# Kernel tuning notes

Measured on AMD Instinct MI355X. Metric: run time of the kernel, lower is better.

Reference implementation:

```python
import jax, jax.numpy as jnp
import numpy as np

B, N = 1, 768
CM, CP = 384, 128            # msa_channel (single repr), pair_channel
H, SQK, SV, PQK, PV = 12, 16, 16, 4, 8
NOUT = 384
NFIN = H * SV + H * PV * 4 + H * CP  # 2112
FP16_HUGE = 65504.0
DIST_EPS = 1e-8


def _quat_to_rot(q):
    # normalized quaternion [B,N,4] -> rotation matrix [B,N,3,3]
    q = q / jnp.sqrt(jnp.sum(q * q, axis=-1, keepdims=True))
    w, x, y, z = q[..., 0], q[..., 1], q[..., 2], q[..., 3]
    return jnp.stack([
        jnp.stack([1 - 2 * (y * y + z * z), 2 * (x * y - w * z), 2 * (x * z + w * y)], -1),
        jnp.stack([2 * (x * y + w * z), 1 - 2 * (x * x + z * z), 2 * (y * z - w * x)], -1),
        jnp.stack([2 * (x * z - w * y), 2 * (y * z + w * x), 1 - 2 * (x * x + y * y)], -1),
    ], -2)


def setup_inputs() -> dict:
    key = jax.random.key(0)
    ks = jax.random.split(key, 20)
    s = 0.02
    return {
        'inputs_1d': jax.random.normal(ks[0], (B, N, CM), jnp.float32),
        'inputs_2d': jax.random.normal(ks[1], (B, N, N, CP), jnp.float32),
        'mask': jnp.ones((B, N, 1), jnp.float32),
        'quat': jax.random.normal(ks[2], (B, N, 4), jnp.float32),
        'trans': jax.random.normal(ks[3], (B, N, 3), jnp.float32),
        'wq': jax.random.normal(ks[4], (CM, H * SQK), jnp.float32) * s,
        'bq': jnp.zeros((H * SQK,), jnp.float32),
        'wkv': jax.random.normal(ks[5], (CM, H * (SQK + SV)), jnp.float32) * s,
        'bkv': jnp.zeros((H * (SQK + SV),), jnp.float32),
        'wqp': jax.random.normal(ks[6], (CM, H * 3 * PQK), jnp.float32) * s,
        'bqp': jnp.zeros((H * 3 * PQK,), jnp.float32),
        'wkvp': jax.random.normal(ks[7], (CM, H * 3 * (PQK + PV)), jnp.float32) * s,
        'bkvp': jnp.zeros((H * 3 * (PQK + PV),), jnp.float32),
        'pw_raw': jnp.full((H,), 0.541323855, jnp.float32),
        'w2d': jax.random.normal(ks[8], (CP, H), jnp.float32) * s,
        'b2d': jnp.zeros((H,), jnp.float32),
        'wout': jax.random.normal(ks[9], (NFIN, NOUT), jnp.float32) * s,
        'bout': jnp.zeros((NOUT,), jnp.float32),
    }


def _ipa(inputs_1d, inputs_2d, mask, quat, trans,
         wq, bq, wkv, bkv, wqp, bqp, wkvp, bkvp, pw_raw, w2d, b2d, wout, bout):
    R = _quat_to_rot(quat)                      # [B,N,3,3]

    # --- scalar q/k/v ---
    q_s = (inputs_1d @ wq + bq).reshape(B, N, H, SQK)
    kv_s = (inputs_1d @ wkv + bkv).reshape(B, N, H, SQK + SV)
    k_s, v_s = kv_s[..., :SQK], kv_s[..., SQK:]

    # --- point q/k/v in global frame: R @ p_local + t ---
    qp = (inputs_1d @ wqp + bqp).reshape(B, N, 3, H * PQK)  # split order: x,y,z blocks
    qp_g = jnp.einsum('bnij,bnjp->bnip', R, qp) + trans[..., None]
    kvp = (inputs_1d @ wkvp + bkvp).reshape(B, N, 3, H * (PQK + PV))
    kvp_g = (jnp.einsum('bnij,bnjp->bnip', R, kvp) + trans[..., None]
             ).reshape(B, N, 3, H, PQK + PV)
    kp_g, vp_g = kvp_g[..., :PQK], kvp_g[..., PQK:]

    # --- attention weights ---
    scalar_w = (1.0 / (3.0 * SQK)) ** 0.5
    point_w = ((1.0 / (3.0 * PQK * 4.5)) ** 0.5) * jax.nn.softplus(pw_raw)  # [H]

    # point-distance logits: -0.5*w_h * sum_{xyz,p} (q-k)^2, via |q|^2+|k|^2-2qk
    q_pt = jnp.transpose(qp_g.reshape(B, N, 3, H, PQK), (0, 3, 1, 2, 4)).reshape(B, H, N, 3 * PQK)
    k_pt = jnp.transpose(kp_g, (0, 3, 1, 2, 4)).reshape(B, H, N, 3 * PQK)
    qq = jnp.sum(q_pt * q_pt, -1)               # [B,H,N]
    kk = jnp.sum(k_pt * k_pt, -1)
    cross = jnp.einsum('bhnd,bhmd->bhnm', q_pt, k_pt)
    attn_pt = -0.5 * point_w[None, :, None, None] * (
        qq[..., :, None] + kk[..., None, :] - 2.0 * cross)

    attn_sc = jnp.einsum('bnhd,bmhd->bhnm', q_s * scalar_w, k_s)
    a2d = jnp.transpose(inputs_2d @ w2d + b2d, (0, 3, 1, 2)) * (1.0 / 3.0) ** 0.5

    logits = attn_sc + attn_pt + a2d
    mask2d = mask * jnp.swapaxes(mask, -1, -2)  # [B,N,N]
    logits = logits - FP16_HUGE * (1.0 - mask2d[:, None])
    attn = jax.nn.softmax(logits, axis=-1)      # [B,H,N,N]

    # --- aggregation ---
    res_s = jnp.einsum('bhnm,bmhd->bnhd', attn, v_s).reshape(B, N, H * SV)
    v_pt = jnp.transpose(vp_g, (0, 3, 1, 2, 4)).reshape(B, H, N, 3 * PV)
    res_pt_g = jnp.einsum('bhnm,bhmd->bhnd', attn, v_pt).reshape(B, H, N, 3, PV)
    res_pt_g = jnp.transpose(res_pt_g, (0, 2, 3, 1, 4)).reshape(B, N, 3, H * PV)
    # invert point: R^T (g - t)
    res_pt_l = jnp.einsum('bnji,bnjp->bnip', R, res_pt_g - trans[..., None])  # [B,N,3,H*PV]
    pt_norm = jnp.sqrt(DIST_EPS + jnp.sum(res_pt_l * res_pt_l, axis=2))       # [B,N,H*PV]
    res_2d = jnp.einsum('bhnm,bnmc->bnhc', attn, inputs_2d).reshape(B, N, H * CP)

    final = jnp.concatenate(
        [res_s, res_pt_l[:, :, 0], res_pt_l[:, :, 1], res_pt_l[:, :, 2], pt_norm, res_2d], -1)
    return final @ wout + bout


def reference(inputs_1d, inputs_2d, mask, quat, trans,
              wq, bq, wkv, bkv, wqp, bqp, wkvp, bkvp, pw_raw, w2d, b2d, wout, bout):
    return _ipa(inputs_1d, inputs_2d, mask, quat, trans,
                wq, bq, wkv, bkv, wqp, bqp, wkvp, bkvp, pw_raw, w2d, b2d, wout, bout)
```

## Files before the change

### kernel.cpp

```cpp
#include <hip/hip_runtime.h>
#include <cstdint>
#include <cstddef>

static constexpr float SCALAR_W = 0.14433756729740643f;
static constexpr float PTW_C    = 0.13608276348795434f;
static constexpr float RSQRT3   = 0.5773502691896258f;
static constexpr float FP16HUGE = 65504.0f;

static constexpr size_t OFF_P    = 0;
static constexpr size_t OFF_R    = 884736;
static constexpr size_t OFF_QPG  = 891648;
static constexpr size_t OFF_KVPG = 1002240;
static constexpr size_t OFF_LG   = 1334016;
static constexpr size_t OFF_FIN  = 8633088;
static constexpr size_t OFF_VCAT = 10255104;
static constexpr size_t OFF_KST  = 10623744;
static constexpr size_t OFF_KPT  = 10771200;
static constexpr size_t WS_TOTAL = 10881792;

__global__ void k_sentinel(float* __restrict__ out, int nel, float val)
{
    const int i = blockIdx.x * 256 + threadIdx.x;
    if (i < nel) out[i] = val;
}

__global__ __launch_bounds__(256) void k_proj_all(const float* __restrict__ A,
    const float* __restrict__ wq,  const float* __restrict__ bq,
    const float* __restrict__ wkv, const float* __restrict__ bkv,
    const float* __restrict__ wqp, const float* __restrict__ bqp,
    const float* __restrict__ wkvp,const float* __restrict__ bkvp,
    float* __restrict__ P)
{
    const int z = blockIdx.z;
    const float* Bm; const float* bias; int ncols, colbase;
    switch (z) {
        case 0: Bm = wq;   bias = bq;   ncols = 192; colbase = 0;   break;
        case 1: Bm = wkv;  bias = bkv;  ncols = 384; colbase = 192; break;
        case 2: Bm = wqp;  bias = bqp;  ncols = 144; colbase = 576; break;
        default:Bm = wkvp; bias = bkvp; ncols = 432; colbase = 720; break;
    }
    if (blockIdx.x * 256 >= ncols) return;
    __shared__ float At[8][384];
    const int t = threadIdx.x;
    const int r0 = blockIdx.y * 8;
    const float4* A4 = reinterpret_cast<const float4*>(A + (size_t)r0 * 384);
    float4* At4 = reinterpret_cast<float4*>(&At[0][0]);
#pragma unroll
    for (int i = 0; i < 3; ++i) At4[t + 256 * i] = A4[t + 256 * i];
    __syncthreads();
    const int col = blockIdx.x * 256 + t;
    if (col >= ncols) return;
    float acc[8] = {0.f,0.f,0.f,0.f,0.f,0.f,0.f,0.f};
    const float* bp = Bm + col;
#pragma unroll 4
    for (int k = 0; k < 384; ++k) {
        const float b = bp[(size_t)k * ncols];
#pragma unroll
        for (int r = 0; r < 8; ++r) acc[r] += At[r][k] * b;
    }
    const float bb = bias[col];
#pragma unroll
    for (int r = 0; r < 8; ++r)
        P[(size_t)(r0 + r) * 1152 + colbase + col] = acc[r] + bb;
}

__global__ __launch_bounds__(256) void k_rmat(const float* __restrict__ quat,
    float* __restrict__ ws)
{
    const int o = blockIdx.x * 256 + threadIdx.x;
    if (o >= 768 * 9) return;
    const int n = o / 9, e = o - 9 * n;
    const float q0 = quat[n*4+0], q1 = quat[n*4+1], q2 = quat[n*4+2], q3 = quat[n*4+3];
    const float inv = 1.0f / sqrtf(q0*q0 + q1*q1 + q2*q2 + q3*q3);
    const float w = q0*inv, x = q1*inv, y = q2*inv, z = q3*inv;
    float R[9];
    R[0] = 1.f - 2.f*(y*y + z*z); R[1] = 2.f*(x*y - w*z); R[2] = 2.f*(x*z + w*y);
    R[3] = 2.f*(x*y + w*z); R[4] = 1.f - 2.f*(x*x + z*z); R[5] = 2.f*(y*z - w*x);
    R[6] = 2.f*(x*z - w*y); R[7] = 2.f*(y*z + w*x); R[8] = 1.f - 2.f*(x*x + y*y);
    ws[OFF_R + o] = R[e];
}

__global__ __launch_bounds__(256) void k_rigid(const float* __restrict__ trans,
    float* __restrict__ ws)
{
    const int o = blockIdx.x * 256 + threadIdx.x;
    if (o >= 768 * 576) return;
    const int n = o / 576, e = o - 576 * n;
    const float* R = ws + OFF_R + (size_t)n * 9;
    if (e < 144) {
        const int i = e / 48, p = e - 48 * i;
        const float* Pn = ws + OFF_P + (size_t)n * 1152 + 576;
        ws[OFF_QPG + (size_t)n*144 + e] =
            R[i*3+0]*Pn[p] + R[i*3+1]*Pn[48+p] + R[i*3+2]*Pn[96+p] + trans[n*3+i];
    } else {
        const int e2 = e - 144;
        const int i = e2 / 144, p = e2 - 144 * i;
        const float* Pn = ws + OFF_P + (size_t)n * 1152 + 720;
        ws[OFF_KVPG + (size_t)n*432 + e2] =
            R[i*3+0]*Pn[p] + R[i*3+1]*Pn[144+p] + R[i*3+2]*Pn[288+p] + trans[n*3+i];
    }
}

__global__ __launch_bounds__(256) void k_vk(float* __restrict__ ws)
{
    const int o = blockIdx.x * 256 + threadIdx.x;
    if (o < 768 * 480) {
        const int m = o / 480, q = o - 480 * m;
        float v;
        if (q < 192) {
            const int h = q >> 4, d = q & 15;
            v = ws[OFF_P + (size_t)m*1152 + 192 + h*32 + 16 + d];
        } else {
            const int q2 = q - 192;
            const int i = q2 / 96, r = q2 - 96*i, h = r >> 3, c = r & 7;
            v = ws[OFF_KVPG + (size_t)m*432 + i*144 + h*12 + 4 + c];
        }
        ws[OFF_VCAT + o] = v;
    } else {
        const int o2 = o - 768 * 480;
        if (o2 >= 768 * 336) return;
        const int m = o2 / 336, q = o2 - 336 * m;
        if (q < 192) {
            const int h = q >> 4, k = q & 15;
            ws[OFF_KST + (size_t)(h*16 + k)*768 + m] =
                ws[OFF_P + (size_t)m*1152 + 192 + h*32 + k];
        } else {
            const int d2 = q - 192;
            const int h = d2 / 12, d = d2 - 12 * h;
            const int i = d >> 2, a = d & 3;
            ws[OFF_KPT + (size_t)(h*12 + d)*768 + m] =
                ws[OFF_KVPG + (size_t)m*432 + i*144 + h*12 + a];
        }
    }
}

__global__ __launch_bounds__(256) void k_lga(const float* __restrict__ in2d,
    const float* __restrict__ w2d, const float* __restrict__ b2d,
    const float* __restrict__ maskp, const float* __restrict__ pw_raw,
    float* __restrict__ ws)
{
    __shared__ float w2l[1536];
    __shared__ float a2l[12][260];
    __shared__ float qs[192], qpl[144], pwl[12], b2l[12];
    const int n = blockIdx.x, mt = blockIdx.y, t = threadIdx.x;
    if (t < 192) qs[t] = ws[OFF_P + (size_t)n*1152 + t] * SCALAR_W;
    if (t < 144) qpl[t] = ws[OFF_QPG + (size_t)n*144 + t];
    if (t < 12) {
        pwl[t] = PTW_C * logf(1.f + expf(pw_raw[t]));
        b2l[t] = b2d[t];
    }
    for (int i = t; i < 1536; i += 256) w2l[i] = w2d[i];
    const float mask_n = maskp[n];
    __syncthreads();

    const int cg = t & 3, pr = t >> 2;
    const int cg4 = cg * 4;
#pragma unroll
    for (int half = 0; half < 4; ++half) {
        const int mm = half * 64 + pr;
        const int m = mt * 256 + mm;
        const float* p = in2d + ((size_t)n * 768 + m) * 128;
        float acc[12] = {0,0,0,0,0,0,0,0,0,0,0,0};
#pragma unroll
        for (int cq = 0; cq < 8; ++cq) {
            const float4 v = *reinterpret_cast<const float4*>(p + cq * 16 + cg4);
#pragma unroll
            for (int j = 0; j < 4; ++j) {
                const float x = (&v.x)[j];
                const int c = cq * 16 + cg4 + j;
#pragma unroll
                for (int h = 0; h < 12; ++h) acc[h] += x * w2l[c * 12 + h];
            }
        }
#pragma unroll
        for (int h = 0; h < 12; ++h) {
            acc[h] += __shfl_xor(acc[h], 1);
            acc[h] += __shfl_xor(acc[h], 2);
        }
        if (cg == 0) {
#pragma unroll
            for (int h = 0; h < 12; ++h)
                a2l[h][mm] = (acc[h] + b2l[h]) * RSQRT3;
        }
    }
    __syncthreads();

    const float* kst = ws + OFF_KST;
    const float* kpt = ws + OFF_KPT;
    const int m = mt * 256 + t;
    const float pen = FP16HUGE * (1.f - mask_n * maskp[m]);
#pragma unroll
    for (int h = 0; h < 12; ++h) {
        float sc = 0.f;
        const float* ks = kst + (size_t)(h*16)*768 + m;
#pragma unroll
        for (int k = 0; k < 16; ++k) sc += qs[h*16 + k] * ks[(size_t)k*768];
        float d2 = 0.f;
        const float* kp = kpt + (size_t)(h*12)*768 + m;
#pragma unroll
        for (int d = 0; d < 12; ++d) {
            const int ii = d >> 2, a = d & 3;
            const float dq = qpl[ii*48 + h*4 + a] - kp[(size_t)d*768];
            d2 += dq * dq;
        }
        ws[OFF_LG + ((size_t)n * 12 + h) * 768 + m] =
            sc - 0.5f * pwl[h] * d2 - pen + a2l[h][t];
    }
}

__global__ __launch_bounds__(512) void k_att(const float* __restrict__ in2d,
    const float* __restrict__ trans, float* __restrict__ ws)
{
    __shared__ float at[12][776];
    __shared__ float part[4][1536];
    __shared__ float fl[480];
    __shared__ float ptl[288];
    __shared__ float Rl[9], trl[3];
    const int n = blockIdx.x, t = threadIdx.x;
    const int wv = t >> 6, lane = t & 63;
    if (t < 9) Rl[t] = ws[OFF_R + n*9 + t];
    if (t < 3) trl[t] = trans[n*3 + t];
    {
        const float4* a4 = reinterpret_cast<const float4*>(ws + OFF_LG + (size_t)n * 9216);
        for (int i = t; i < 2304; i += 512) {
            const int row = i / 192, j = i - row * 192;
            *reinterpret_cast<float4*>(&at[row][j * 4]) = a4[i];
        }
    }
    __syncthreads();

    for (int h = wv; h < 12; h += 8) {
        float v[12];
        float mx = -3.0e38f;
#pragma unroll
        for (int i = 0; i < 12; ++i) { v[i] = at[h][lane + i*64]; mx = fmaxf(mx, v[i]); }
#pragma unroll
        for (int off = 32; off > 0; off >>= 1) mx = fmaxf(mx, __shfl_xor(mx, off));
        float s = 0.f;
#pragma unroll
        for (int i = 0; i < 12; ++i) { v[i] = expf(v[i] - mx); s += v[i]; }
#pragma unroll
        for (int off = 32; off > 0; off >>= 1) s += __shfl_xor(s, off);
        const float inv = 1.f / s;
#pragma unroll
        for (int i = 0; i < 12; ++i) at[h][lane + i*64] = v[i] * inv;
    }
    __syncthreads();

    {
        const int c = t & 127, g = t >> 7;
        const float* p = in2d + (size_t)n * 768 * 128 + c;
        float acc[12] = {0,0,0,0,0,0,0,0,0,0,0,0};
        const int m0 = g * 192;
#pragma unroll 4
        for (int m = m0; m < m0 + 192; ++m) {
            const float x = p[(size_t)m * 128];
#pragma unroll
            for (int h = 0; h < 12; ++h) acc[h] += at[h][m] * x;
        }
#pragma unroll
        for (int h = 0; h < 12; ++h) part[g][h * 128 + c] = acc[h];
    }
    __syncthreads();
    {
        float* fo = ws + OFF_FIN + (size_t)n * 2112 + 576;
        for (int o = t; o < 1536; o += 512)
            fo[o] = part[0][o] + part[1][o] + part[2][o] + part[3][o];
    }

    if (t < 480) {
        int h;
        if (t < 192) h = t >> 4;
        else { const int r = (t - 192) % 96; h = r >> 3; }
        const float* v = ws + OFF_VCAT + t;
        const float* a = &at[h][0];
        float s = 0.f;
        for (int m = 0; m < 768; ++m) s += a[m] * v[(size_t)m * 480];
        fl[t] = s;
    }
    __syncthreads();

    float* fo = ws + OFF_FIN + (size_t)n * 2112;
    if (t < 192) fo[t] = fl[t];
    if (t < 288) {
        const int i = t / 96, p = t - 96 * i;
        float s = 0.f;
#pragma unroll
        for (int j = 0; j < 3; ++j)
            s += Rl[j*3 + i] * (fl[192 + j*96 + p] - trl[j]);
        fo[192 + t] = s;
        ptl[t] = s;
    }
    __syncthreads();
    if (t < 96) {
        const float a = ptl[t], b = ptl[96 + t], c = ptl[192 + t];
        fo[480 + t] = sqrtf(1e-8f + a*a + b*b + c*c);
    }
}

__global__ __launch_bounds__(256) void k_final(const float* __restrict__ wout,
    const float* __restrict__ bout, const float* __restrict__ ws,
    float* __restrict__ out)
{
    __shared__ float At[8][64];
    __shared__ float Bt[64][132];
    const float* fin = ws + OFF_FIN;
    const int r0 = blockIdx.y * 8;
    const int c0 = blockIdx.x * 128;
    const int t = threadIdx.x;
    const int c = t & 127, half = t >> 7;
    float acc[4] = {0.f, 0.f, 0.f, 0.f};
    for (int k0 = 0; k0 < 2112; k0 += 64) {
        __syncthreads();
        if (t < 128) {
            const int r = t >> 4, j = t & 15;
            *reinterpret_cast<float4*>(&At[r][j * 4]) =
                *reinterpret_cast<const float4*>(&fin[(size_t)(r0 + r) * 2112 + k0 + j * 4]);
        }
#pragma unroll
        for (int i = t; i < 2048; i += 256) {
            const int k = i >> 5, j = i & 31;
            *reinterpret_cast<float4*>(&Bt[k][j * 4]) =
                *reinterpret_cast<const float4*>(&wout[(size_t)(k0 + k) * 384 + c0 + j * 4]);
        }
        __syncthreads();
#pragma unroll
        for (int k = 0; k < 64; ++k) {
            const float b = Bt[k][c];
#pragma unroll
            for (int r = 0; r < 4; ++r) acc[r] += At[half*4 + r][k] * b;
        }
    }
#pragma unroll
    for (int r = 0; r < 4; ++r)
        out[(size_t)(r0 + half*4 + r) * 384 + c0 + c] = acc[r] + bout[c0 + c];
}

extern "C" void kernel_launch(void* const* d_in, const int* in_sizes, int n_in,
                              void* d_out, int out_size, void* d_ws, size_t ws_size,
                              hipStream_t stream)
{
    const float* in1d  = (const float*)d_in[0];
    const float* in2d  = (const float*)d_in[1];
    const float* maskp = (const float*)d_in[2];
    const float* quat  = (const float*)d_in[3];
    const float* trans = (const float*)d_in[4];
    const float* wq    = (const float*)d_in[5];
    const float* bq    = (const float*)d_in[6];
    const float* wkv   = (const float*)d_in[7];
    const float* bkv   = (const float*)d_in[8];
    const float* wqp   = (const float*)d_in[9];
    const float* bqp   = (const float*)d_in[10];
    const float* wkvp  = (const float*)d_in[11];
    const float* bkvp  = (const float*)d_in[12];
    const float* pwr   = (const float*)d_in[13];
    const float* w2d   = (const float*)d_in[14];
    const float* b2d   = (const float*)d_in[15];
    const float* wout  = (const float*)d_in[16];
    const float* bout  = (const float*)d_in[17];
    float* ws  = (float*)d_ws;
    float* out = (float*)d_out;

    if (ws_size < WS_TOTAL * sizeof(float)) {
        const float val = 1000.0f + (float)(ws_size / (1024.0 * 1024.0));
        k_sentinel<<<dim3((out_size + 255) / 256), dim3(256), 0, stream>>>(out, out_size, val);
        return;
    }

    dim3 blk(256);
    k_proj_all<<<dim3(2, 96, 4), blk, 0, stream>>>(in1d, wq, bq, wkv, bkv,
                                                   wqp, bqp, wkvp, bkvp, ws);
    k_rmat<<<dim3((768*9 + 255)/256), blk, 0, stream>>>(quat, ws);
    k_rigid<<<dim3((768*576 + 255)/256), blk, 0, stream>>>(trans, ws);
    k_vk<<<dim3((768*816 + 255)/256), blk, 0, stream>>>(ws);
    k_lga<<<dim3(768, 3), blk, 0, stream>>>(in2d, w2d, b2d, maskp, pwr, ws);
    k_att<<<dim3(768), dim3(512), 0, stream>>>(in2d, trans, ws);
    k_final<<<dim3(3, 96), blk, 0, stream>>>(wout, bout, ws, out);
}
```

Measured before the change: 495.2 us.

## Fuse logit computation into attention kernel, removing the logits workspace round trip

Merges the kernel that builds attention logits (pair bias, scalar and point terms) into the softmax/aggregation kernel, one block per query row with 512 threads. Logits are written straight into shared memory instead of a global buffer that was written and then re-read, and one kernel launch goes away. The cost is fewer blocks for the logit phase (768 instead of 2304) and higher shared-memory use per block, which may lower occupancy. The 2d input row of the same query is now read twice within one block, so the second read may hit in cache.

Result: slower. 932.7 us (+88.3%).

```diff
diff --git a/kernel.cpp b/kernel.cpp
--- a/kernel.cpp
+++ b/kernel.cpp
@@ -11,7 +11,6 @@
 static constexpr size_t OFF_R    = 884736;
 static constexpr size_t OFF_QPG  = 891648;
 static constexpr size_t OFF_KVPG = 1002240;
-static constexpr size_t OFF_LG   = 1334016;
 static constexpr size_t OFF_FIN  = 8633088;
 static constexpr size_t OFF_VCAT = 10255104;
 static constexpr size_t OFF_KST  = 10623744;
@@ -134,97 +133,87 @@
     }
 }
 
-__global__ __launch_bounds__(256) void k_lga(const float* __restrict__ in2d,
+__global__ __launch_bounds__(512) void k_fused(const float* __restrict__ in2d,
     const float* __restrict__ w2d, const float* __restrict__ b2d,
     const float* __restrict__ maskp, const float* __restrict__ pw_raw,
-    float* __restrict__ ws)
-{
+    const float* __restrict__ trans, float* __restrict__ ws)
+{
+    __shared__ float at[12][776];
+    __shared__ float part[4][1536];
     __shared__ float w2l[1536];
-    __shared__ float a2l[12][260];
     __shared__ float qs[192], qpl[144], pwl[12], b2l[12];
-    const int n = blockIdx.x, mt = blockIdx.y, t = threadIdx.x;
+    __shared__ float fl[480];
+    __shared__ float ptl[288];
+    __shared__ float Rl[9], trl[3];
+    const int n = blockIdx.x, t = threadIdx.x;
+    const int wv = t >> 6, lane = t & 63;
+
     if (t < 192) qs[t] = ws[OFF_P + (size_t)n*1152 + t] * SCALAR_W;
     if (t < 144) qpl[t] = ws[OFF_QPG + (size_t)n*144 + t];
     if (t < 12) {
         pwl[t] = PTW_C * logf(1.f + expf(pw_raw[t]));
         b2l[t] = b2d[t];
     }
-    for (int i = t; i < 1536; i += 256) w2l[i] = w2d[i];
-    const float mask_n = maskp[n];
-    __syncthreads();
-
-    const int cg = t & 3, pr = t >> 2;
-    const int cg4 = cg * 4;
-#pragma unroll
-    for (int half = 0; half < 4; ++half) {
-        const int mm = half * 64 + pr;
-        const int m = mt * 256 + mm;
-        const float* p = in2d + ((size_t)n * 768 + m) * 128;
-        float acc[12] = {0,0,0,0,0,0,0,0,0,0,0,0};
-#pragma unroll
-        for (int cq = 0; cq < 8; ++cq) {
-            const float4 v = *reinterpret_cast<const float4*>(p + cq * 16 + cg4);
-#pragma unroll
-            for (int j = 0; j < 4; ++j) {
-                const float x = (&v.x)[j];
-                const int c = cq * 16 + cg4 + j;
-#pragma unroll
-                for (int h = 0; h < 12; ++h) acc[h] += x * w2l[c * 12 + h];
-            }
-        }
-#pragma unroll
-        for (int h = 0; h < 12; ++h) {
-            acc[h] += __shfl_xor(acc[h], 1);
-            acc[h] += __shfl_xor(acc[h], 2);
-        }
-        if (cg == 0) {
-#pragma unroll
-            for (int h = 0; h < 12; ++h)
-                a2l[h][mm] = (acc[h] + b2l[h]) * RSQRT3;
-        }
-    }
-    __syncthreads();
-
-    const float* kst = ws + OFF_KST;
-    const float* kpt = ws + OFF_KPT;
-    const int m = mt * 256 + t;
-    const float pen = FP16HUGE * (1.f - mask_n * maskp[m]);
-#pragma unroll
-    for (int h = 0; h < 12; ++h) {
-        float sc = 0.f;
-        const float* ks = kst + (size_t)(h*16)*768 + m;
-#pragma unroll
-        for (int k = 0; k < 16; ++k) sc += qs[h*16 + k] * ks[(size_t)k*768];
-        float d2 = 0.f;
-        const float* kp = kpt + (size_t)(h*12)*768 + m;
-#pragma unroll
-        for (int d = 0; d < 12; ++d) {
-            const int ii = d >> 2, a = d & 3;
-            const float dq = qpl[ii*48 + h*4 + a] - kp[(size_t)d*768];
-            d2 += dq * dq;
-        }
-        ws[OFF_LG + ((size_t)n * 12 + h) * 768 + m] =
-            sc - 0.5f * pwl[h] * d2 - pen + a2l[h][t];
-    }
-}
-
-__global__ __launch_bounds__(512) void k_att(const float* __restrict__ in2d,
-    const float* __restrict__ trans, float* __restrict__ ws)
-{
-    __shared__ float at[12][776];
-    __shared__ float part[4][1536];
-    __shared__ float fl[480];
-    __shared__ float ptl[288];
-    __shared__ float Rl[9], trl[3];
-    const int n = blockIdx.x, t = threadIdx.x;
-    const int wv = t >> 6, lane = t & 63;
     if (t < 9) Rl[t] = ws[OFF_R + n*9 + t];
     if (t < 3) trl[t] = trans[n*3 + t];
+    for (int i = t; i < 1536; i += 512) w2l[i] = w2d[i];
+    const float mask_n = maskp[n];
+    __syncthreads();
+
     {
-        const float4* a4 = reinterpret_cast<const float4*>(ws + OFF_LG + (size_t)n * 9216);
-        for (int i = t; i < 2304; i += 512) {
-            const int row = i / 192, j = i - row * 192;
-            *reinterpret_cast<float4*>(&at[row][j * 4]) = a4[i];
+        const int cg = t & 3, pr = t >> 2;
+        const int cg4 = cg * 4;
+#pragma unroll 1
+        for (int r = 0; r < 6; ++r) {
+            const int m = r * 128 + pr;
+            const float* p = in2d + ((size_t)n * 768 + m) * 128;
+            float acc[12] = {0,0,0,0,0,0,0,0,0,0,0,0};
+#pragma unroll
+            for (int cq = 0; cq < 8; ++cq) {
+                const float4 v = *reinterpret_cast<const float4*>(p + cq * 16 + cg4);
+#pragma unroll
+                for (int j = 0; j < 4; ++j) {
+                    const float x = (&v.x)[j];
+                    const float* wr = &w2l[(cq * 16 + cg4 + j) * 12];
+#pragma unroll
+                    for (int h = 0; h < 12; ++h) acc[h] += x * wr[h];
+                }
+            }
+#pragma unroll
+            for (int h = 0; h < 12; ++h) {
+                acc[h] += __shfl_xor(acc[h], 1);
+                acc[h] += __shfl_xor(acc[h], 2);
+            }
+            if (cg == 0) {
+#pragma unroll
+                for (int h = 0; h < 12; ++h)
+                    at[h][m] = (acc[h] + b2l[h]) * RSQRT3;
+            }
+        }
+    }
+    __syncthreads();
+
+    {
+        const float* kst = ws + OFF_KST;
+        const float* kpt = ws + OFF_KPT;
+        for (int m = t; m < 768; m += 512) {
+            const float pen = FP16HUGE * (1.f - mask_n * maskp[m]);
+#pragma unroll
+            for (int h = 0; h < 12; ++h) {
+                float sc = 0.f;
+                const float* ks = kst + (size_t)(h*16)*768 + m;
+#pragma unroll
+                for (int k = 0; k < 16; ++k) sc += qs[h*16 + k] * ks[(size_t)k*768];
+                float d2 = 0.f;
+                const float* kp = kpt + (size_t)(h*12)*768 + m;
+#pragma unroll
+                for (int d = 0; d < 12; ++d) {
+                    const int ii = d >> 2, a = d & 3;
+                    const float dq = qpl[ii*48 + h*4 + a] - kp[(size_t)d*768];
+                    d2 += dq * dq;
+                }
+                at[h][m] += sc - 0.5f * pwl[h] * d2 - pen;
+            }
         }
     }
     __syncthreads();
@@ -373,7 +362,7 @@
     k_rmat<<<dim3((768*9 + 255)/256), blk, 0, stream>>>(quat, ws);
     k_rigid<<<dim3((768*576 + 255)/256), blk, 0, stream>>>(trans, ws);
     k_vk<<<dim3((768*816 + 255)/256), blk, 0, stream>>>(ws);
-    k_lga<<<dim3(768, 3), blk, 0, stream>>>(in2d, w2d, b2d, maskp, pwr, ws);
-    k_att<<<dim3(768), dim3(512), 0, stream>>>(in2d, trans, ws);
+    k_fused<<<dim3(768), dim3(512), 0, stream>>>(in2d, w2d, b2d, maskp, pwr,
+                                                 trans, ws);
     k_final<<<dim3(3, 96), blk, 0, stream>>>(wout, bout, ws, out);
 }
```

## Split logits kernel into reuse-tiled q·k/point-distance pass and pair-bias pass

Applied to the files above, without the earlier changes.

The fused logits kernel is split in two. k_log computes the scalar q·k and point-distance terms for 8 query rows per block, keeping each key column's 16 scalar and 12 point values in registers and reusing them across those 8 rows. This cuts global reads of the transposed key tensors by a factor of eight. k_a2d then streams the pair representation and adds the 2D bias into the logits with a read-modify-write, which costs an extra kernel launch and one more pass over the logits buffer.

New measurement: 495.6 us. No clear change (+0.1%).

```diff
diff --git a/kernel.cpp b/kernel.cpp
--- a/kernel.cpp
+++ b/kernel.cpp
@@ -134,23 +134,67 @@
     }
 }
 
-__global__ __launch_bounds__(256) void k_lga(const float* __restrict__ in2d,
+__global__ __launch_bounds__(256) void k_log(const float* __restrict__ maskp,
+    const float* __restrict__ pw_raw, float* __restrict__ ws)
+{
+    __shared__ float qsl[8][192], qpl8[8][144], pwl[12], mskn[8];
+    const int nt = blockIdx.x, mt = blockIdx.y, t = threadIdx.x;
+    const int n0 = nt * 8;
+    for (int idx = t; idx < 1536; idx += 256) {
+        const int i = idx / 192, j = idx - i * 192;
+        qsl[i][j] = ws[OFF_P + (size_t)(n0 + i) * 1152 + j] * SCALAR_W;
+    }
+    for (int idx = t; idx < 1152; idx += 256) {
+        const int i = idx / 144, j = idx - i * 144;
+        qpl8[i][j] = ws[OFF_QPG + (size_t)(n0 + i) * 144 + j];
+    }
+    if (t < 12) pwl[t] = PTW_C * logf(1.f + expf(pw_raw[t]));
+    if (t < 8) mskn[t] = maskp[n0 + t];
+    __syncthreads();
+
+    const int m = mt * 128 + (t & 127);
+    const int h0 = (t >> 7) * 6;
+    const float mask_m = maskp[m];
+    const float* kst = ws + OFF_KST;
+    const float* kpt = ws + OFF_KPT;
+#pragma unroll 1
+    for (int hh = 0; hh < 6; ++hh) {
+        const int h = h0 + hh;
+        float xk[16];
+#pragma unroll
+        for (int k = 0; k < 16; ++k) xk[k] = kst[(size_t)(h*16 + k)*768 + m];
+        float xd[12];
+#pragma unroll
+        for (int d = 0; d < 12; ++d) xd[d] = kpt[(size_t)(h*12 + d)*768 + m];
+        const float pw = pwl[h];
+#pragma unroll
+        for (int i = 0; i < 8; ++i) {
+            float sc = 0.f;
+#pragma unroll
+            for (int k = 0; k < 16; ++k) sc += qsl[i][h*16 + k] * xk[k];
+            float d2 = 0.f;
+#pragma unroll
+            for (int d = 0; d < 12; ++d) {
+                const int ii = d >> 2, a = d & 3;
+                const float dq = qpl8[i][ii*48 + h*4 + a] - xd[d];
+                d2 += dq * dq;
+            }
+            const float pen = FP16HUGE * (1.f - mskn[i] * mask_m);
+            ws[OFF_LG + ((size_t)(n0 + i) * 12 + h) * 768 + m] =
+                sc - 0.5f * pw * d2 - pen;
+        }
+    }
+}
+
+__global__ __launch_bounds__(256) void k_a2d(const float* __restrict__ in2d,
     const float* __restrict__ w2d, const float* __restrict__ b2d,
-    const float* __restrict__ maskp, const float* __restrict__ pw_raw,
     float* __restrict__ ws)
 {
     __shared__ float w2l[1536];
-    __shared__ float a2l[12][260];
-    __shared__ float qs[192], qpl[144], pwl[12], b2l[12];
+    __shared__ float b2l[12];
     const int n = blockIdx.x, mt = blockIdx.y, t = threadIdx.x;
-    if (t < 192) qs[t] = ws[OFF_P + (size_t)n*1152 + t] * SCALAR_W;
-    if (t < 144) qpl[t] = ws[OFF_QPG + (size_t)n*144 + t];
-    if (t < 12) {
-        pwl[t] = PTW_C * logf(1.f + expf(pw_raw[t]));
-        b2l[t] = b2d[t];
-    }
+    if (t < 12) b2l[t] = b2d[t];
     for (int i = t; i < 1536; i += 256) w2l[i] = w2d[i];
-    const float mask_n = maskp[n];
     __syncthreads();
 
     const int cg = t & 3, pr = t >> 2;
@@ -167,9 +211,9 @@
 #pragma unroll
             for (int j = 0; j < 4; ++j) {
                 const float x = (&v.x)[j];
-                const int c = cq * 16 + cg4 + j;
-#pragma unroll
-                for (int h = 0; h < 12; ++h) acc[h] += x * w2l[c * 12 + h];
+                const float* wr = &w2l[(cq * 16 + cg4 + j) * 12];
+#pragma unroll
+                for (int h = 0; h < 12; ++h) acc[h] += x * wr[h];
             }
         }
 #pragma unroll
@@ -178,33 +222,11 @@
             acc[h] += __shfl_xor(acc[h], 2);
         }
         if (cg == 0) {
+            float* lgp = ws + OFF_LG + (size_t)n * 9216 + m;
 #pragma unroll
             for (int h = 0; h < 12; ++h)
-                a2l[h][mm] = (acc[h] + b2l[h]) * RSQRT3;
-        }
-    }
-    __syncthreads();
-
-    const float* kst = ws + OFF_KST;
-    const float* kpt = ws + OFF_KPT;
-    const int m = mt * 256 + t;
-    const float pen = FP16HUGE * (1.f - mask_n * maskp[m]);
-#pragma unroll
-    for (int h = 0; h < 12; ++h) {
-        float sc = 0.f;
-        const float* ks = kst + (size_t)(h*16)*768 + m;
-#pragma unroll
-        for (int k = 0; k < 16; ++k) sc += qs[h*16 + k] * ks[(size_t)k*768];
-        float d2 = 0.f;
-        const float* kp = kpt + (size_t)(h*12)*768 + m;
-#pragma unroll
-        for (int d = 0; d < 12; ++d) {
-            const int ii = d >> 2, a = d & 3;
-            const float dq = qpl[ii*48 + h*4 + a] - kp[(size_t)d*768];
-            d2 += dq * dq;
-        }
-        ws[OFF_LG + ((size_t)n * 12 + h) * 768 + m] =
-            sc - 0.5f * pwl[h] * d2 - pen + a2l[h][t];
+                lgp[(size_t)h * 768] += (acc[h] + b2l[h]) * RSQRT3;
+        }
     }
 }
 
@@ -373,7 +395,8 @@
     k_rmat<<<dim3((768*9 + 255)/256), blk, 0, stream>>>(quat, ws);
     k_rigid<<<dim3((768*576 + 255)/256), blk, 0, stream>>>(trans, ws);
     k_vk<<<dim3((768*816 + 255)/256), blk, 0, stream>>>(ws);
-    k_lga<<<dim3(768, 3), blk, 0, stream>>>(in2d, w2d, b2d, maskp, pwr, ws);
+    k_log<<<dim3(96, 6), blk, 0, stream>>>(maskp, pwr, ws);
+    k_a2d<<<dim3(768, 3), blk, 0, stream>>>(in2d, w2d, b2d, ws);
     k_att<<<dim3(768), dim3(512), 0, stream>>>(in2d, trans, ws);
     k_final<<<dim3(3, 96), blk, 0, stream>>>(wout, bout, ws, out);
 }
```
